# Performance work log

Hardware: AMD Instinct MI355X
Metric: run time of the kernel (lower is better)

## Reference

```python
import jax, jax.numpy as jnp
import numpy as np

LEAKY = 0.2  # negative_slope of self.act / apply_non_linearity

def setup_inputs() -> dict:
    key = jax.random.key(0)
    ks = jax.random.split(key, 9)
    N_HOP, B, M, D = 2, 2048, 32, 32
    ENT, REL, ITEM, USER = 500000, 200, 100000, 100000
    return {
        "pos_items": jax.random.randint(ks[0], (B,), 0, ITEM),
        "memories_h": jax.random.randint(ks[1], (N_HOP, B, M), 0, ENT),
        "memories_r": jax.random.randint(ks[2], (N_HOP, B, M), 0, REL),
        "memories_t": jax.random.randint(ks[3], (N_HOP, B, M), 0, ENT),
        "uEmbed": jax.random.normal(ks[4], (USER, D), jnp.float32) * 0.1,
        "iEmbed": jax.random.normal(ks[5], (ITEM, D), jnp.float32) * 0.1,
        "entity_emb": jax.random.normal(ks[6], (ENT, D), jnp.float32) * 0.1,
        "relation_emb": jax.random.normal(ks[7], (REL, D * D), jnp.float32) * 0.1,
        "transform_W": jax.random.normal(ks[8], (D, D), jnp.float32) * 0.1,
    }

def reference(pos_items, memories_h, memories_r, memories_t,
              uEmbed, iEmbed, entity_emb, relation_emb, transform_W):
    D = uEmbed.shape[1]
    n_hop = memories_h.shape[0]
    # hop-stacked embedding gathers
    h_all = entity_emb[memories_h]                                   # [H,B,M,D]
    r_all = relation_emb[memories_r].reshape(*memories_r.shape, D, D)  # [H,B,M,D,D]
    t_all = jax.nn.leaky_relu(entity_emb[memories_t], negative_slope=LEAKY)  # [H,B,M,D]
    # _key_addressing, starting from gathered item embeddings
    item = iEmbed[pos_items]                                         # [B,D]
    for hop in range(n_hop):
        Rh = jnp.einsum('bmde,bme->bmd', r_all[hop], h_all[hop])     # R @ h per memory slot
        probs = jax.nn.softmax(jnp.einsum('bmd,bd->bm', Rh, item), axis=1)
        o = jnp.einsum('bm,bmd->bd', probs, t_all[hop])              # weighted sum of tails
        item = (item + o) @ transform_W.T                            # plus_transform update
    # in-place scatter under torch.no_grad(): value has no grad path
    iEmbed_new = iEmbed + jax.lax.stop_gradient(iEmbed.at[pos_items].set(item) - iEmbed)
    return (uEmbed, iEmbed_new, h_all, t_all, r_all)
```

## Files before the change

### kernel.cpp

```cpp
#include <hip/hip_runtime.h>

#define LEAKY 0.2f

constexpr int H = 2, B = 2048, M = 32, Dd = 32;
constexpr int NSLOT = H * B * M;

typedef float f32x4 __attribute__((ext_vector_type(4)));

__global__ void copy_ui_kernel(const f32x4* __restrict__ u,
                               const f32x4* __restrict__ it,
                               f32x4* __restrict__ out_u,
                               f32x4* __restrict__ out_i, int n4) {
    int i = blockIdx.x * blockDim.x + threadIdx.x;
    if (i < n4) {
        f32x4 uv = __builtin_nontemporal_load(&u[i]);
        f32x4 iv = __builtin_nontemporal_load(&it[i]);
        __builtin_nontemporal_store(uv, &out_u[i]);
        __builtin_nontemporal_store(iv, &out_i[i]);
    }
}

__global__ void winner_kernel(const int* __restrict__ pos,
                              int* __restrict__ winner, int n) {
    int i = blockIdx.x * blockDim.x + threadIdx.x;
    if (i < n) atomicMax(&winner[pos[i]], i);
}

__global__ __launch_bounds__(256) void gather_kernel(
    const int* __restrict__ mh, const int* __restrict__ mr,
    const int* __restrict__ mt, const float* __restrict__ ent,
    const float* __restrict__ rel, float* __restrict__ out_h,
    float* __restrict__ out_t, float* __restrict__ out_r,
    float* __restrict__ Rh) {
    int tid  = blockIdx.x * blockDim.x + threadIdx.x;
    int s    = tid >> 6;
    int lane = threadIdx.x & 63;
    if (s >= NSLOT) return;

    int hidx = mh[s], ridx = mr[s], tidx = mt[s];

    const f32x4* src = (const f32x4*)(rel + (size_t)ridx * (Dd * Dd));
    f32x4*       dst = (f32x4*)(out_r + (size_t)s * (Dd * Dd));

    int e0 = (lane * 4) & 31;
    f32x4 hv = __builtin_nontemporal_load(
        (const f32x4*)(ent + (size_t)hidx * Dd + e0));

    float partial[4];
#pragma unroll
    for (int k = 0; k < 4; k++) {
        f32x4 v = src[lane + 64 * k];
        __builtin_nontemporal_store(v, &dst[lane + 64 * k]);
        partial[k] = v.x * hv.x + v.y * hv.y + v.z * hv.z + v.w * hv.w;
    }
#pragma unroll
    for (int off = 1; off < 8; off <<= 1) {
#pragma unroll
        for (int k = 0; k < 4; k++)
            partial[k] += __shfl_xor(partial[k], off, 64);
    }
    if ((lane & 7) == 0) {
        int dbase = lane >> 3;
#pragma unroll
        for (int k = 0; k < 4; k++)
            Rh[(size_t)s * Dd + dbase + 8 * k] = partial[k];
    }
    if (lane < 8) {
        __builtin_nontemporal_store(hv, &((f32x4*)(out_h + (size_t)s * Dd))[lane]);
        f32x4 tv = __builtin_nontemporal_load(
            (const f32x4*)(ent + (size_t)tidx * Dd + lane * 4));
        tv.x = tv.x > 0.f ? tv.x : LEAKY * tv.x;
        tv.y = tv.y > 0.f ? tv.y : LEAKY * tv.y;
        tv.z = tv.z > 0.f ? tv.z : LEAKY * tv.z;
        tv.w = tv.w > 0.f ? tv.w : LEAKY * tv.w;
        ((f32x4*)(out_t + (size_t)s * Dd))[lane] = tv;
    }
}

__global__ __launch_bounds__(64) void ripple_kernel(
    const int* __restrict__ pos_items, const float* __restrict__ iEmbed,
    const float* __restrict__ W, const float* __restrict__ Rh,
    const float* __restrict__ t_all, const int* __restrict__ winner,
    float* __restrict__ out_i) {
    int b = blockIdx.x;
    int lane = threadIdx.x;
    int m = lane & 31, half = lane >> 5;

    __shared__ float item[32], pv[32], pre[32];

    int pos = pos_items[b];
    if (lane < 32) item[lane] = iEmbed[(size_t)pos * Dd + lane];
    __syncthreads();

    for (int hop = 0; hop < H; hop++) {
        const float* Rhb = Rh    + (size_t)(hop * B + b) * M * Dd;
        const float* tb  = t_all + (size_t)(hop * B + b) * M * Dd;

        float partial = 0.f;
        for (int e = half * 16; e < half * 16 + 16; e++)
            partial += Rhb[m * Dd + e] * item[e];
        partial += __shfl_xor(partial, 32, 64);

        float mx = partial;
#pragma unroll
        for (int msk = 16; msk >= 1; msk >>= 1)
            mx = fmaxf(mx, __shfl_xor(mx, msk, 64));
        float ex = __expf(partial - mx);
        float sm = ex;
#pragma unroll
        for (int msk = 16; msk >= 1; msk >>= 1)
            sm += __shfl_xor(sm, msk, 64);
        float p = ex / sm;

        if (lane < 32) pv[lane] = p;
        __syncthreads();

        float po = 0.f;
        for (int mm = half * 16; mm < half * 16 + 16; mm++)
            po += pv[mm] * tb[mm * Dd + m];
        po += __shfl_xor(po, 32, 64);
        float newpre = item[m] + po;
        __syncthreads();
        if (lane < 32) pre[lane] = newpre;
        __syncthreads();

        float r = 0.f;
        for (int e = half * 16; e < half * 16 + 16; e++)
            r += pre[e] * W[m * Dd + e];
        r += __shfl_xor(r, 32, 64);
        __syncthreads();
        if (lane < 32) item[lane] = r;
        __syncthreads();
    }

    if (winner[pos] == b && lane < 32)
        out_i[(size_t)pos * Dd + lane] = item[lane];
}

extern "C" void kernel_launch(void* const* d_in, const int* in_sizes, int n_in,
                              void* d_out, int out_size, void* d_ws, size_t ws_size,
                              hipStream_t stream) {
    const int*   pos_items   = (const int*)d_in[0];
    const int*   memories_h  = (const int*)d_in[1];
    const int*   memories_r  = (const int*)d_in[2];
    const int*   memories_t  = (const int*)d_in[3];
    const float* uEmbed      = (const float*)d_in[4];
    const float* iEmbed      = (const float*)d_in[5];
    const float* entity_emb  = (const float*)d_in[6];
    const float* relation_emb= (const float*)d_in[7];
    const float* transform_W = (const float*)d_in[8];

    const int n_user_elems = in_sizes[4];
    const int n_item_elems = in_sizes[5];
    const int n_items      = n_item_elems / Dd;

    float* out_u = (float*)d_out;
    float* out_i = out_u + n_user_elems;
    float* out_h = out_i + n_item_elems;
    float* out_t = out_h + (size_t)NSLOT * Dd;
    float* out_r = out_t + (size_t)NSLOT * Dd;

    int*   winner = (int*)d_ws;
    float* Rh     = (float*)((char*)d_ws + 512 * 1024);

    (void)hipMemsetAsync(winner, 0xFF, (size_t)n_items * sizeof(int), stream);

    {
        int n4 = n_user_elems / 4;
        int blocks = (n4 + 255) / 256;
        copy_ui_kernel<<<blocks, 256, 0, stream>>>(
            (const f32x4*)uEmbed, (const f32x4*)iEmbed,
            (f32x4*)out_u, (f32x4*)out_i, n4);
    }

    winner_kernel<<<(B + 255) / 256, 256, 0, stream>>>(pos_items, winner, B);

    {
        int waves_per_block = 4;
        int blocks = NSLOT / waves_per_block;
        gather_kernel<<<blocks, 256, 0, stream>>>(
            memories_h, memories_r, memories_t, entity_emb, relation_emb,
            out_h, out_t, out_r, Rh);
    }

    ripple_kernel<<<B, 64, 0, stream>>>(pos_items, iEmbed, transform_W,
                                        Rh, out_t, winner, out_i);
}
```

Before: 701.1 us.

## Split gather into grid-stride relation copy with Rh and separate h/t gather kernel

After: 720.2 us. 1.03x slower.

```diff
diff --git a/kernel.cpp b/kernel.cpp
--- a/kernel.cpp
+++ b/kernel.cpp
@@ -4,6 +4,13 @@
 
 constexpr int H = 2, B = 2048, M = 32, Dd = 32;
 constexpr int NSLOT = H * B * M;
+constexpr int N4_R  = NSLOT * 64;
+
+constexpr int RCOPY_N4      = NSLOT * 256;
+constexpr int RCOPY_BLOCKS  = 2048;
+constexpr int RCOPY_THREADS = 256;
+constexpr int RCOPY_STRIDE  = RCOPY_BLOCKS * RCOPY_THREADS;
+constexpr int RCOPY_ITERS   = RCOPY_N4 / RCOPY_STRIDE;
 
 typedef float f32x4 __attribute__((ext_vector_type(4)));
 
@@ -26,55 +33,57 @@
     if (i < n) atomicMax(&winner[pos[i]], i);
 }
 
-__global__ __launch_bounds__(256) void gather_kernel(
-    const int* __restrict__ mh, const int* __restrict__ mr,
-    const int* __restrict__ mt, const float* __restrict__ ent,
-    const float* __restrict__ rel, float* __restrict__ out_h,
-    float* __restrict__ out_t, float* __restrict__ out_r,
-    float* __restrict__ Rh) {
-    int tid  = blockIdx.x * blockDim.x + threadIdx.x;
-    int s    = tid >> 6;
-    int lane = threadIdx.x & 63;
-    if (s >= NSLOT) return;
+__global__ __launch_bounds__(RCOPY_THREADS) void rcopy_rh_kernel(
+    const int* __restrict__ mr, const int* __restrict__ mh,
+    const float* __restrict__ ent, const float* __restrict__ rel,
+    float* __restrict__ out_r, float* __restrict__ Rh) {
+    const int tid  = blockIdx.x * RCOPY_THREADS + threadIdx.x;
+    const int lane = threadIdx.x & 63;
+    const int e0   = (lane * 4) & 31;
+    const f32x4* rel4 = (const f32x4*)rel;
+    f32x4*       out4 = (f32x4*)out_r;
 
-    int hidx = mh[s], ridx = mr[s], tidx = mt[s];
+#pragma unroll 4
+    for (int it = 0; it < RCOPY_ITERS; ++it) {
+        int j = tid + it * RCOPY_STRIDE;
+        int slot = __builtin_amdgcn_readfirstlane(j >> 8);
+        int o    = j & 255;
+        int ridx = mr[slot];
+        int hidx = mh[slot];
 
-    const f32x4* src = (const f32x4*)(rel + (size_t)ridx * (Dd * Dd));
-    f32x4*       dst = (f32x4*)(out_r + (size_t)s * (Dd * Dd));
+        f32x4 v = rel4[(size_t)ridx * 256 + o];
+        __builtin_nontemporal_store(v, &out4[j]);
 
-    int e0 = (lane * 4) & 31;
-    f32x4 hv = __builtin_nontemporal_load(
-        (const f32x4*)(ent + (size_t)hidx * Dd + e0));
+        f32x4 hv = *(const f32x4*)(ent + (size_t)hidx * Dd + e0);
+        float partial = v.x * hv.x + v.y * hv.y + v.z * hv.z + v.w * hv.w;
+#pragma unroll
+        for (int off = 1; off < 8; off <<= 1)
+            partial += __shfl_xor(partial, off, 64);
+        if ((lane & 7) == 0) {
+            int d = o >> 3;
+            Rh[(size_t)slot * Dd + d] = partial;
+        }
+    }
+}
 
-    float partial[4];
-#pragma unroll
-    for (int k = 0; k < 4; k++) {
-        f32x4 v = src[lane + 64 * k];
-        __builtin_nontemporal_store(v, &dst[lane + 64 * k]);
-        partial[k] = v.x * hv.x + v.y * hv.y + v.z * hv.z + v.w * hv.w;
-    }
-#pragma unroll
-    for (int off = 1; off < 8; off <<= 1) {
-#pragma unroll
-        for (int k = 0; k < 4; k++)
-            partial[k] += __shfl_xor(partial[k], off, 64);
-    }
-    if ((lane & 7) == 0) {
-        int dbase = lane >> 3;
-#pragma unroll
-        for (int k = 0; k < 4; k++)
-            Rh[(size_t)s * Dd + dbase + 8 * k] = partial[k];
-    }
-    if (lane < 8) {
-        __builtin_nontemporal_store(hv, &((f32x4*)(out_h + (size_t)s * Dd))[lane]);
-        f32x4 tv = __builtin_nontemporal_load(
-            (const f32x4*)(ent + (size_t)tidx * Dd + lane * 4));
-        tv.x = tv.x > 0.f ? tv.x : LEAKY * tv.x;
-        tv.y = tv.y > 0.f ? tv.y : LEAKY * tv.y;
-        tv.z = tv.z > 0.f ? tv.z : LEAKY * tv.z;
-        tv.w = tv.w > 0.f ? tv.w : LEAKY * tv.w;
-        ((f32x4*)(out_t + (size_t)s * Dd))[lane] = tv;
-    }
+__global__ __launch_bounds__(256) void ht_gather_kernel(
+    const int* __restrict__ mh, const int* __restrict__ mt,
+    const float* __restrict__ ent, float* __restrict__ out_h,
+    float* __restrict__ out_t) {
+    int i = blockIdx.x * blockDim.x + threadIdx.x;
+    int slot = i >> 3, o = i & 7;
+    int hidx = mh[slot], tidx = mt[slot];
+    const f32x4* ent4 = (const f32x4*)ent;
+
+    f32x4 hv = __builtin_nontemporal_load(&ent4[(size_t)hidx * 8 + o]);
+    __builtin_nontemporal_store(hv, &((f32x4*)out_h)[i]);
+
+    f32x4 tv = __builtin_nontemporal_load(&ent4[(size_t)tidx * 8 + o]);
+    tv.x = tv.x > 0.f ? tv.x : LEAKY * tv.x;
+    tv.y = tv.y > 0.f ? tv.y : LEAKY * tv.y;
+    tv.z = tv.z > 0.f ? tv.z : LEAKY * tv.z;
+    tv.w = tv.w > 0.f ? tv.w : LEAKY * tv.w;
+    ((f32x4*)out_t)[i] = tv;
 }
 
 __global__ __launch_bounds__(64) void ripple_kernel(
@@ -175,13 +184,11 @@
 
     winner_kernel<<<(B + 255) / 256, 256, 0, stream>>>(pos_items, winner, B);
 
-    {
-        int waves_per_block = 4;
-        int blocks = NSLOT / waves_per_block;
-        gather_kernel<<<blocks, 256, 0, stream>>>(
-            memories_h, memories_r, memories_t, entity_emb, relation_emb,
-            out_h, out_t, out_r, Rh);
-    }
+    rcopy_rh_kernel<<<RCOPY_BLOCKS, RCOPY_THREADS, 0, stream>>>(
+        memories_r, memories_h, entity_emb, relation_emb, out_r, Rh);
+
+    ht_gather_kernel<<<NSLOT * 8 / 256, 256, 0, stream>>>(
+        memories_h, memories_t, entity_emb, out_h, out_t);
 
     ripple_kernel<<<B, 64, 0, stream>>>(pos_items, iEmbed, transform_W,
                                         Rh, out_t, winner, out_i);
```
